# Kernel tuning notes

Hardware: AMD Instinct MI355X
Metric: run time of the kernel (lower is better)

Reference implementation:

```python
import jax, jax.numpy as jnp
import numpy as np

B = 8
H1c = W1c = 56
H2c = W2c = 112
C1 = 512
C2 = 256
NH = 8
WS = 7
POOL = 2
EPS = 1e-5


def setup_inputs() -> dict:
    key = jax.random.key(0)
    ks = jax.random.split(key, 8)
    x = jax.random.normal(ks[0], (B, H1c * W1c, C1), dtype=jnp.float32)
    y = jax.random.normal(ks[1], (B, H2c * W2c, C2), dtype=jnp.float32)
    Wq = jax.random.normal(ks[2], (C1, C1), dtype=jnp.float32) * 0.02
    Wkv = jax.random.normal(ks[3], (2 * C1, C2), dtype=jnp.float32) * 0.02
    Wproj = jax.random.normal(ks[4], (C1, C1), dtype=jnp.float32) * 0.02
    bproj = jnp.zeros((C1,), dtype=jnp.float32)
    # 1x1 conv: fan_out = out_channels -> std = sqrt(2/C2)
    Wsr = jax.random.normal(ks[5], (C2, C2), dtype=jnp.float32) * np.sqrt(2.0 / C2).astype(np.float32)
    bsr = jnp.zeros((C2,), dtype=jnp.float32)
    gn = jnp.ones((C2,), dtype=jnp.float32)
    bn = jnp.zeros((C2,), dtype=jnp.float32)
    return {"x": x, "y": y, "Wq": Wq, "Wkv": Wkv, "Wproj": Wproj,
            "bproj": bproj, "Wsr": Wsr, "bsr": bsr, "gn": gn, "bn": bn,
            "H1": H1c, "W1": W1c, "H2": H2c, "W2": W2c}


def _window_partition(t, ws):
    # t: (B, nh, H, W, C) -> (B*nh, num_windows, ws*ws, C)
    Bt, n, H, W, C = t.shape
    ht, wt = H // ws, W // ws
    t = t.reshape(Bt, n, ht, ws, wt, ws, C).transpose(0, 1, 2, 4, 3, 5, 6)
    return t.reshape(Bt * n, ht * wt, ws * ws, C)


def reference(x, y, Wq, Wkv, Wproj, bproj, Wsr, bsr, gn, bn, H1, W1, H2, W2):
    B1, N1, c1 = x.shape
    B2, N2, c2 = y.shape
    nh, ws = NH, WS
    hd = c1 // nh
    scale = hd ** (-0.5)

    # q projection -> (B, nh, H1, W1, hd)
    q = (x @ Wq.T).reshape(B1, H1, W1, nh, hd).transpose(0, 3, 1, 2, 4)

    # KV preprocessing: avgpool -> 1x1 conv -> layernorm -> gelu
    y2 = y.transpose(0, 2, 1).reshape(B2, c2, H2, W2)
    Hp, Wp = H2 // POOL, W2 // POOL
    y2 = y2.reshape(B2, c2, Hp, POOL, Wp, POOL).mean(axis=(3, 5))
    y2 = jnp.einsum('bchw,oc->bohw', y2, Wsr) + bsr[None, :, None, None]
    y2 = y2.reshape(B2, c2, Hp * Wp).transpose(0, 2, 1)  # (B, Np, C2)
    mu = y2.mean(-1, keepdims=True)
    var = y2.var(-1, keepdims=True)
    y2 = (y2 - mu) / jnp.sqrt(var + EPS) * gn + bn
    y2 = jax.nn.gelu(y2, approximate=False)

    kv = (y2 @ Wkv.T).reshape(B2, Hp * Wp, 2, nh, hd)
    k = kv[:, :, 0].transpose(0, 2, 1, 3).reshape(B2, nh, Hp, Wp, hd)
    v = kv[:, :, 1].transpose(0, 2, 1, 3).reshape(B2, nh, Hp, Wp, hd)

    qw = _window_partition(q, ws)   # (B*nh, nw, ws^2, hd)
    kw = _window_partition(k, ws)
    vw = _window_partition(v, ws)

    attn = jax.nn.softmax(jnp.einsum('bnqd,bnkd->bnqk', qw, kw) * scale, axis=-1)
    out = jnp.einsum('bnqk,bnkd->bnqd', attn, vw)  # (B*nh, nw, ws^2, hd)

    # window reverse -> (B, N1, C1)
    ht, wt = H1 // ws, W1 // ws
    out = out.reshape(B1, nh, ht, wt, ws, ws, hd).transpose(0, 1, 2, 4, 3, 5, 6)
    out = out.reshape(B1, nh, H1 * W1, hd).transpose(0, 2, 1, 3).reshape(B1, H1 * W1, c1)
    return out @ Wproj.T + bproj
```

## Files before the change

### kernel.cpp

```cpp
#include <hip/hip_runtime.h>
#include <hip/hip_bf16.h>

typedef __attribute__((ext_vector_type(8))) short short8;
typedef __attribute__((ext_vector_type(4))) float f32x4;
typedef __attribute__((ext_vector_type(4))) unsigned short ushort4v;

#define DI __device__ __forceinline__

DI unsigned short f2bf(float f) {
  union { float f; unsigned int u; } a; a.f = f;
  unsigned int u = a.u;
  return (unsigned short)((u + 0x7FFFu + ((u >> 16) & 1u)) >> 16);
}

#define BARRIER() do { asm volatile("" ::: "memory"); __builtin_amdgcn_s_barrier(); asm volatile("" ::: "memory"); } while (0)
#define GLOAD16(src, dst) __builtin_amdgcn_global_load_lds( \
    (const __attribute__((address_space(1))) void*)(src), \
    (__attribute__((address_space(3))) void*)(dst), 16, 0, 0)


__global__ __launch_bounds__(256)
void cvt_pool(const float* __restrict__ y, unsigned short* __restrict__ pooled,
              const float* __restrict__ Wq, const float* __restrict__ Wkv,
              const float* __restrict__ Wproj, const float* __restrict__ Wsr,
              unsigned short* __restrict__ Wq_b, unsigned short* __restrict__ Wkv_b,
              unsigned short* __restrict__ Wproj_b, unsigned short* __restrict__ Wsr_b) {
  int bid = blockIdx.x;
  if (bid < 6272) {
    int t = bid * 256 + threadIdx.x;
    int cv = (t & 63) * 4;
    int bp = t >> 6;
    int b = bp / 3136, p = bp % 3136;
    int hp = p / 56, wp = p % 56;
    const float* src = y + (((size_t)b * 12544) + hp * 224 + wp * 2) * 256 + cv;
    float4 a0 = *(const float4*)(src);
    float4 a1 = *(const float4*)(src + 256);
    float4 a2 = *(const float4*)(src + 28672);
    float4 a3 = *(const float4*)(src + 28672 + 256);
    float4 av;
    av.x = (a0.x + a1.x + a2.x + a3.x) * 0.25f;
    av.y = (a0.y + a1.y + a2.y + a3.y) * 0.25f;
    av.z = (a0.z + a1.z + a2.z + a3.z) * 0.25f;
    av.w = (a0.w + a1.w + a2.w + a3.w) * 0.25f;
    ushort4v o = { f2bf(av.x), f2bf(av.y), f2bf(av.z), f2bf(av.w) };
    *(ushort4v*)&pooled[(size_t)bp * 256 + cv] = o;
  } else {
    long i = (long)(bid - 6272) * 1024 + threadIdx.x * 4;
    const float* src; unsigned short* dst; long off;
    if (i < 262144L)      { src = Wq;    dst = Wq_b;    off = i; }
    else if (i < 524288L) { src = Wkv;   dst = Wkv_b;   off = i - 262144L; }
    else if (i < 786432L) { src = Wproj; dst = Wproj_b; off = i - 524288L; }
    else                  { src = Wsr;   dst = Wsr_b;   off = i - 786432L; }
    float4 v = *(const float4*)&src[off];
    ushort4v o = { f2bf(v.x), f2bf(v.y), f2bf(v.z), f2bf(v.w) };
    *(ushort4v*)&dst[off] = o;
  }
}

__global__ __launch_bounds__(256)
void sr_gemm(const unsigned short* __restrict__ Ap, const unsigned short* __restrict__ Wsr_b,
             const float* __restrict__ bsr, const float* __restrict__ gn,
             const float* __restrict__ bn, unsigned short* __restrict__ out) {
  __shared__ unsigned short sA[64 * 64];
  __shared__ unsigned short sB[256 * 64];
  __shared__ float red[64 * 8];

  const int tid = threadIdx.x;
  const int wv = tid >> 6;
  const int lane = tid & 63;
  const int lr = lane & 15;
  const int lg = lane >> 4;
  const int lr4 = lg * 4;
  const int m0 = blockIdx.x * 64;
  const int sr8 = lane >> 3;
  const int sl8 = lane & 7;

  f32x4 acc[4][4];
#pragma unroll
  for (int i = 0; i < 4; ++i)
#pragma unroll
    for (int j = 0; j < 4; ++j) acc[i][j] = (f32x4){0.f, 0.f, 0.f, 0.f};

  for (int kt = 0; kt < 256; kt += 64) {
#pragma unroll
    for (int c = 0; c < 2; ++c) {
      int row = wv * 16 + c * 8 + sr8;
      GLOAD16(Ap + (size_t)(m0 + row) * 256 + kt + ((sl8 ^ (row & 7)) * 8),
              &sA[(wv * 16 + c * 8) * 64]);
    }
#pragma unroll
    for (int c = 0; c < 8; ++c) {
      int row = wv * 64 + c * 8 + sr8;
      GLOAD16(Wsr_b + (size_t)row * 256 + kt + ((sl8 ^ (row & 7)) * 8),
              &sB[(wv * 64 + c * 8) * 64]);
    }
    __syncthreads();
#pragma unroll
    for (int ks = 0; ks < 2; ++ks) {
      short8 af[4], bfr[4];
#pragma unroll
      for (int i = 0; i < 4; ++i)
        af[i] = *(const short8*)&sA[(i * 16 + lr) * 64 + (((ks * 4 + lg) ^ (lr & 7)) * 8)];
#pragma unroll
      for (int j = 0; j < 4; ++j)
        bfr[j] = *(const short8*)&sB[(wv * 64 + j * 16 + lr) * 64 + (((ks * 4 + lg) ^ (lr & 7)) * 8)];
#pragma unroll
      for (int i = 0; i < 4; ++i)
#pragma unroll
        for (int j = 0; j < 4; ++j)
          acc[i][j] = __builtin_amdgcn_mfma_f32_16x16x32_bf16(af[i], bfr[j], acc[i][j], 0, 0, 0);
    }
    __syncthreads();
  }

  float bsv[4], gnv[4], bnv[4];
#pragma unroll
  for (int j = 0; j < 4; ++j) {
    int col = wv * 64 + j * 16 + lr;
    bsv[j] = bsr[col]; gnv[j] = gn[col]; bnv[j] = bn[col];
  }
  float s_[4][4], q_[4][4];
#pragma unroll
  for (int i = 0; i < 4; ++i)
#pragma unroll
    for (int r = 0; r < 4; ++r) {
      float s = 0.f, q = 0.f;
#pragma unroll
      for (int j = 0; j < 4; ++j) {
        float v = acc[i][j][r] + bsv[j];
        acc[i][j][r] = v;
        s += v; q += v * v;
      }
      s_[i][r] = s; q_[i][r] = q;
    }
#pragma unroll
  for (int m = 1; m <= 8; m <<= 1)
#pragma unroll
    for (int i = 0; i < 4; ++i)
#pragma unroll
      for (int r = 0; r < 4; ++r) {
        s_[i][r] += __shfl_xor(s_[i][r], m);
        q_[i][r] += __shfl_xor(q_[i][r], m);
      }
  if (lr == 0) {
#pragma unroll
    for (int i = 0; i < 4; ++i)
#pragma unroll
      for (int r = 0; r < 4; ++r) {
        int row = i * 16 + lr4 + r;
        red[row * 8 + wv * 2 + 0] = s_[i][r];
        red[row * 8 + wv * 2 + 1] = q_[i][r];
      }
  }
  __syncthreads();
#pragma unroll
  for (int i = 0; i < 4; ++i) {
#pragma unroll
    for (int r = 0; r < 4; ++r) {
      int row = i * 16 + lr4 + r;
      float sum = red[row * 8 + 0] + red[row * 8 + 2] + red[row * 8 + 4] + red[row * 8 + 6];
      float sq  = red[row * 8 + 1] + red[row * 8 + 3] + red[row * 8 + 5] + red[row * 8 + 7];
      float mean = sum * (1.f / 256.f);
      float var = sq * (1.f / 256.f) - mean * mean;
      float rstd = rsqrtf(var + 1e-5f);
#pragma unroll
      for (int j = 0; j < 4; ++j) {
        float t = (acc[i][j][r] - mean) * rstd * gnv[j] + bnv[j];
        t = 0.5f * t * (1.f + erff(t * 0.70710678118654752f));
        out[(size_t)(m0 + row) * 256 + wv * 64 + j * 16 + lr] = f2bf(t);
      }
    }
  }
}

DI void epi_q(int gm, int gc, float v, unsigned short* outp) {
  const int b = gm / 3136, pos = gm % 3136;
  const int h = pos / 56, ww = pos % 56;
  const int head = gc >> 6, d = gc & 63;
  const size_t idx = ((((size_t)(b * 8 + head)) * 64 + (h / 7) * 8 + (ww / 7)) * 49
                      + (h % 7) * 7 + (ww % 7)) * 64 + d;
  outp[idx] = f2bf(v);
}

template<int K, int N>
__global__ __launch_bounds__(512, 2)
void gemm256f(const float* __restrict__ A,
              const unsigned short* __restrict__ Bw,
              unsigned short* __restrict__ outp) {
  __shared__ unsigned short lds[65536];
  const int tid = threadIdx.x;
  const int wv = tid >> 6;
  const int lane = tid & 63;
  const int wm = wv >> 2;
  const int wn = wv & 3;
  const int m0 = blockIdx.y * 256;
  const int n0 = blockIdx.x * 256;
  const int lr = lane & 15;
  const int lg = lane >> 4;
  const int lr4 = lg * 4;
  const int srow8 = lane >> 3;
  const int sl8 = lane & 7;
  constexpr int NT = K / 64;

  f32x4 acc[8][4];
#pragma unroll
  for (int i = 0; i < 8; ++i)
#pragma unroll
    for (int j = 0; j < 4; ++j) acc[i][j] = (f32x4){0.f, 0.f, 0.f, 0.f};

  float4 fa[4][2];
  auto loadA = [&](int t1) {
    int tsrc = (t1 < NT) ? t1 : NT - 1;
#pragma unroll
    for (int rr = 0; rr < 4; ++rr) {
      int trow = rr * 64 + wv * 8 + srow8;
      const float* p = A + (size_t)(m0 + trow) * K + tsrc * 64 + sl8 * 8;
      fa[rr][0] = *(const float4*)p;
      fa[rr][1] = *(const float4*)(p + 4);
    }
    asm volatile("" ::: "memory");
  };
  auto writeA = [&](int t1) {
#pragma unroll
    for (int rr = 0; rr < 4; ++rr) {
      int trow = rr * 64 + wv * 8 + srow8;
      union { short8 s; unsigned short u[8]; } w;
      w.u[0] = f2bf(fa[rr][0].x); w.u[1] = f2bf(fa[rr][0].y);
      w.u[2] = f2bf(fa[rr][0].z); w.u[3] = f2bf(fa[rr][0].w);
      w.u[4] = f2bf(fa[rr][1].x); w.u[5] = f2bf(fa[rr][1].y);
      w.u[6] = f2bf(fa[rr][1].z); w.u[7] = f2bf(fa[rr][1].w);
      *(short8*)&lds[(t1 & 1) * 32768 + trow * 64 + ((sl8 ^ (trow & 7)) * 8)] = w.s;
    }
  };
  auto stageB = [&](int t1, int rr) {
    int tsrc = (t1 < NT) ? t1 : NT - 1;
    int trow = rr * 64 + wv * 8 + srow8;
    int sx = sl8 ^ (trow & 7);
    GLOAD16(Bw + (size_t)(n0 + trow) * K + tsrc * 64 + sx * 8,
            &lds[(t1 & 1) * 32768 + 16384 + (rr * 64 + wv * 8) * 64]);
  };
  auto rdA = [&](int s, int mf, int ks) -> short8 {
    int row = wm * 128 + mf * 16 + lr;
    int slot = ((ks << 2) + lg) ^ (row & 7);
    return *(const short8*)&lds[s * 32768 + row * 64 + slot * 8];
  };
  auto rdB = [&](int s, int nf, int ks) -> short8 {
    int row = wn * 64 + nf * 16 + lr;
    int slot = ((ks << 2) + lg) ^ (row & 7);
    return *(const short8*)&lds[s * 32768 + 16384 + row * 64 + slot * 8];
  };

  stageB(0, 0); stageB(0, 1); stageB(0, 2); stageB(0, 3);
  loadA(0);
  asm volatile("s_waitcnt vmcnt(0)" ::: "memory");
  writeA(0);
  asm volatile("s_waitcnt lgkmcnt(0)" ::: "memory");
  BARRIER();

  for (int t = 0; t < NT; ++t) {
    const int s = t & 1;
    short8 bfr[4][2];
    loadA(t + 1);
#pragma unroll
    for (int j = 0; j < 4; ++j) { bfr[j][0] = rdB(s, j, 0); bfr[j][1] = rdB(s, j, 1); }
    {
      short8 x0 = rdA(s, 0, 0), x1 = rdA(s, 0, 1);
      short8 y0 = rdA(s, 1, 0), y1 = rdA(s, 1, 1);
      BARRIER();
      __builtin_amdgcn_s_setprio(1);
#pragma unroll
      for (int j = 0; j < 4; ++j) {
        acc[0][j] = __builtin_amdgcn_mfma_f32_16x16x32_bf16(x0, bfr[j][0], acc[0][j], 0, 0, 0);
        acc[0][j] = __builtin_amdgcn_mfma_f32_16x16x32_bf16(x1, bfr[j][1], acc[0][j], 0, 0, 0);
        acc[1][j] = __builtin_amdgcn_mfma_f32_16x16x32_bf16(y0, bfr[j][0], acc[1][j], 0, 0, 0);
        acc[1][j] = __builtin_amdgcn_mfma_f32_16x16x32_bf16(y1, bfr[j][1], acc[1][j], 0, 0, 0);
      }
      __builtin_amdgcn_s_setprio(0);
      BARRIER();
    }
    stageB(t + 1, 0); stageB(t + 1, 1);
    {
      short8 x0 = rdA(s, 2, 0), x1 = rdA(s, 2, 1);
      short8 y0 = rdA(s, 3, 0), y1 = rdA(s, 3, 1);
      BARRIER();
      __builtin_amdgcn_s_setprio(1);
#pragma unroll
      for (int j = 0; j < 4; ++j) {
        acc[2][j] = __builtin_amdgcn_mfma_f32_16x16x32_bf16(x0, bfr[j][0], acc[2][j], 0, 0, 0);
        acc[2][j] = __builtin_amdgcn_mfma_f32_16x16x32_bf16(x1, bfr[j][1], acc[2][j], 0, 0, 0);
        acc[3][j] = __builtin_amdgcn_mfma_f32_16x16x32_bf16(y0, bfr[j][0], acc[3][j], 0, 0, 0);
        acc[3][j] = __builtin_amdgcn_mfma_f32_16x16x32_bf16(y1, bfr[j][1], acc[3][j], 0, 0, 0);
      }
      __builtin_amdgcn_s_setprio(0);
      BARRIER();
    }
    stageB(t + 1, 2); stageB(t + 1, 3);
    {
      short8 x0 = rdA(s, 4, 0), x1 = rdA(s, 4, 1);
      short8 y0 = rdA(s, 5, 0), y1 = rdA(s, 5, 1);
      BARRIER();
      __builtin_amdgcn_s_setprio(1);
#pragma unroll
      for (int j = 0; j < 4; ++j) {
        acc[4][j] = __builtin_amdgcn_mfma_f32_16x16x32_bf16(x0, bfr[j][0], acc[4][j], 0, 0, 0);
        acc[4][j] = __builtin_amdgcn_mfma_f32_16x16x32_bf16(x1, bfr[j][1], acc[4][j], 0, 0, 0);
        acc[5][j] = __builtin_amdgcn_mfma_f32_16x16x32_bf16(y0, bfr[j][0], acc[5][j], 0, 0, 0);
        acc[5][j] = __builtin_amdgcn_mfma_f32_16x16x32_bf16(y1, bfr[j][1], acc[5][j], 0, 0, 0);
      }
      __builtin_amdgcn_s_setprio(0);
      BARRIER();
    }
    {
      short8 x0 = rdA(s, 6, 0), x1 = rdA(s, 6, 1);
      short8 y0 = rdA(s, 7, 0), y1 = rdA(s, 7, 1);
      asm volatile("s_waitcnt vmcnt(4)" ::: "memory");
      writeA(t + 1);
      asm volatile("s_waitcnt lgkmcnt(0)" ::: "memory");
      BARRIER();
      __builtin_amdgcn_s_setprio(1);
#pragma unroll
      for (int j = 0; j < 4; ++j) {
        acc[6][j] = __builtin_amdgcn_mfma_f32_16x16x32_bf16(x0, bfr[j][0], acc[6][j], 0, 0, 0);
        acc[6][j] = __builtin_amdgcn_mfma_f32_16x16x32_bf16(x1, bfr[j][1], acc[6][j], 0, 0, 0);
        acc[7][j] = __builtin_amdgcn_mfma_f32_16x16x32_bf16(y0, bfr[j][0], acc[7][j], 0, 0, 0);
        acc[7][j] = __builtin_amdgcn_mfma_f32_16x16x32_bf16(y1, bfr[j][1], acc[7][j], 0, 0, 0);
      }
      __builtin_amdgcn_s_setprio(0);
      asm volatile("s_waitcnt vmcnt(0)" ::: "memory");
      BARRIER();
    }
  }

#pragma unroll
  for (int i = 0; i < 8; ++i)
#pragma unroll
    for (int j = 0; j < 4; ++j)
#pragma unroll
      for (int r = 0; r < 4; ++r)
        epi_q(m0 + wm * 128 + i * 16 + lr4 + r, n0 + wn * 64 + j * 16 + lr,
              acc[i][j][r], outp);
}

__global__ __launch_bounds__(1024)
void kvattn(const unsigned short* __restrict__ y2,
            const unsigned short* __restrict__ Wkv_b,
            const unsigned short* __restrict__ qwin,
            const unsigned short* __restrict__ Wproj_b,
            const float* __restrict__ bproj,
            float* __restrict__ out) {
  __shared__ unsigned short lds[81920];
  const int tid = threadIdx.x;
  const int wv16 = tid >> 6;
  const int head = wv16 >> 1;
  const int half = wv16 & 1;
  const int lane = tid & 63;
  const int lr = lane & 15;
  const int lg = lane >> 4;
  const int r8 = lane >> 3;
  const int sl8 = lane & 7;
  const int bb = blockIdx.x >> 6;
  const int win = blockIdx.x & 63;
  const int ht = win >> 3, wt = win & 7;

  unsigned short* Cy  = lds;
  unsigned short* SLh = lds + 16384 + head * 8192;
  unsigned short* OA  = lds + 16384;
  unsigned short* WPs = lds + 49152 + wv16 * 2048;

  {
    int rb = wv16 & 7;
    int m = rb * 8 + r8;
    int mm = (m < 49) ? m : 48;
    int grow = bb * 3136 + (ht * 7 + mm / 7) * 56 + wt * 7 + (mm % 7);
    int p0 = wv16 >> 3;
#pragma unroll
    for (int pp = 0; pp < 2; ++pp) {
      int panel = p0 + pp * 2;
      GLOAD16(y2 + (size_t)grow * 256 + panel * 64 + ((sl8 ^ (m & 7)) * 8),
              &Cy[panel * 4096 + rb * 512]);
    }
  }

  auto stageW = [&](int s) {
    int h2 = s >> 2, kt = s & 3;
#pragma unroll
    for (int c = 0; c < 4; ++c) {
      int lrow = half * 32 + c * 8 + r8;
      GLOAD16(Wkv_b + (size_t)(h2 * 512 + head * 64 + lrow) * 256 + kt * 64 + ((sl8 ^ r8) * 8),
              &SLh[(s & 1) * 4096 + (half * 32 + c * 8) * 64]);
    }
  };

  f32x4 aK[4][2], aV[4][2];
#pragma unroll
  for (int i = 0; i < 4; ++i)
#pragma unroll
    for (int j = 0; j < 2; ++j) { aK[i][j] = (f32x4){0,0,0,0}; aV[i][j] = (f32x4){0,0,0,0}; }

  stageW(0);
  asm volatile("s_waitcnt vmcnt(4)" ::: "memory");
  BARRIER();

#pragma unroll
  for (int s = 0; s < 8; ++s) {
    if (s < 7) {
      stageW(s + 1);
      asm volatile("s_waitcnt vmcnt(4)" ::: "memory");
    } else {
      asm volatile("s_waitcnt vmcnt(0)" ::: "memory");
    }
    const int kt = s & 3;
    const unsigned short* Wb = &SLh[(s & 1) * 4096];
    short8 bfrg[2][2];
#pragma unroll
    for (int nf2 = 0; nf2 < 2; ++nf2)
#pragma unroll
      for (int ks = 0; ks < 2; ++ks) {
        int row = (half * 2 + nf2) * 16 + lr;
        bfrg[nf2][ks] = *(const short8*)&Wb[row * 64 + (((ks * 4 + lg) ^ (lr & 7)) * 8)];
      }
#pragma unroll
    for (int mf = 0; mf < 4; ++mf)
#pragma unroll
      for (int ks = 0; ks < 2; ++ks) {
        short8 af = *(const short8*)&Cy[kt * 4096 + (mf * 16 + lr) * 64 + (((ks * 4 + lg) ^ (lr & 7)) * 8)];
#pragma unroll
        for (int nf2 = 0; nf2 < 2; ++nf2) {
          if (s < 4)
            aK[mf][nf2] = __builtin_amdgcn_mfma_f32_16x16x32_bf16(af, bfrg[nf2][ks], aK[mf][nf2], 0, 0, 0);
          else
            aV[mf][nf2] = __builtin_amdgcn_mfma_f32_16x16x32_bf16(af, bfrg[nf2][ks], aV[mf][nf2], 0, 0, 0);
        }
      }
  }

  const unsigned short* qb = qwin + (size_t)((bb * 8 + head) * 64 + win) * 3136;
  short8 qf[2][2];
#pragma unroll
  for (int mf2 = 0; mf2 < 2; ++mf2)
#pragma unroll
    for (int ks = 0; ks < 2; ++ks)
      qf[mf2][ks] = *(const short8*)&qb[((half * 2 + mf2) * 16 + lr) * 64 + ks * 32 + lg * 8];

  BARRIER();

#pragma unroll
  for (int mf = 0; mf < 4; ++mf)
#pragma unroll
    for (int nf2 = 0; nf2 < 2; ++nf2)
#pragma unroll
      for (int r = 0; r < 4; ++r) {
        int key = mf * 16 + lg * 4 + r;
        int d = (half * 2 + nf2) * 16 + lr;
        SLh[key * 64 + (((d >> 3) ^ (key & 7)) * 8) + (d & 7)] = f2bf(aK[mf][nf2][r]);
        SLh[4096 + d * 64 + (((key >> 3) ^ (d & 7)) * 8) + (key & 7)] = f2bf(aV[mf][nf2][r]);
      }
  asm volatile("s_waitcnt lgkmcnt(0)" ::: "memory");
  BARRIER();

  f32x4 aS[2][4];
#pragma unroll
  for (int i = 0; i < 2; ++i)
#pragma unroll
    for (int j = 0; j < 4; ++j) aS[i][j] = (f32x4){0,0,0,0};
#pragma unroll
  for (int mf2 = 0; mf2 < 2; ++mf2)
#pragma unroll
    for (int ks = 0; ks < 2; ++ks)
#pragma unroll
      for (int nf = 0; nf < 4; ++nf) {
        short8 bk = *(const short8*)&SLh[(nf * 16 + lr) * 64 + (((ks * 4 + lg) ^ (lr & 7)) * 8)];
        aS[mf2][nf] = __builtin_amdgcn_mfma_f32_16x16x32_bf16(qf[mf2][ks], bk, aS[mf2][nf], 0, 0, 0);
      }

#pragma unroll
  for (int nf = 0; nf < 4; ++nf)
    if (nf * 16 + lr >= 49) {
#pragma unroll
      for (int mf2 = 0; mf2 < 2; ++mf2)
#pragma unroll
        for (int r = 0; r < 4; ++r) aS[mf2][nf][r] = -1e30f;
    }
  const float cexp = 0.125f * 1.4426950408889634f;
  float mx[2][4], sm[2][4];
#pragma unroll
  for (int mf2 = 0; mf2 < 2; ++mf2)
#pragma unroll
    for (int r = 0; r < 4; ++r)
      mx[mf2][r] = fmaxf(fmaxf(aS[mf2][0][r], aS[mf2][1][r]), fmaxf(aS[mf2][2][r], aS[mf2][3][r]));
#pragma unroll
  for (int m = 1; m <= 8; m <<= 1)
#pragma unroll
    for (int mf2 = 0; mf2 < 2; ++mf2)
#pragma unroll
      for (int r = 0; r < 4; ++r) mx[mf2][r] = fmaxf(mx[mf2][r], __shfl_xor(mx[mf2][r], m));
#pragma unroll
  for (int mf2 = 0; mf2 < 2; ++mf2)
#pragma unroll
    for (int nf = 0; nf < 4; ++nf)
#pragma unroll
      for (int r = 0; r < 4; ++r)
        aS[mf2][nf][r] = exp2f((aS[mf2][nf][r] - mx[mf2][r]) * cexp);
#pragma unroll
  for (int mf2 = 0; mf2 < 2; ++mf2)
#pragma unroll
    for (int r = 0; r < 4; ++r)
      sm[mf2][r] = aS[mf2][0][r] + aS[mf2][1][r] + aS[mf2][2][r] + aS[mf2][3][r];
#pragma unroll
  for (int m = 1; m <= 8; m <<= 1)
#pragma unroll
    for (int mf2 = 0; mf2 < 2; ++mf2)
#pragma unroll
      for (int r = 0; r < 4; ++r) sm[mf2][r] += __shfl_xor(sm[mf2][r], m);
#pragma unroll
  for (int mf2 = 0; mf2 < 2; ++mf2)
#pragma unroll
    for (int r = 0; r < 4; ++r) sm[mf2][r] = 1.f / sm[mf2][r];

  BARRIER();

#pragma unroll
  for (int mf2 = 0; mf2 < 2; ++mf2)
#pragma unroll
    for (int nf = 0; nf < 4; ++nf)
#pragma unroll
      for (int r = 0; r < 4; ++r) {
        int q = (half * 2 + mf2) * 16 + lg * 4 + r;
        int key = nf * 16 + lr;
        SLh[q * 64 + (((key >> 3) ^ (q & 7)) * 8) + (key & 7)] = f2bf(aS[mf2][nf][r] * sm[mf2][r]);
      }

  f32x4 aO[2][4];
#pragma unroll
  for (int i = 0; i < 2; ++i)
#pragma unroll
    for (int j = 0; j < 4; ++j) aO[i][j] = (f32x4){0,0,0,0};
#pragma unroll
  for (int mf2 = 0; mf2 < 2; ++mf2)
#pragma unroll
    for (int ks = 0; ks < 2; ++ks) {
      int qrow = (half * 2 + mf2) * 16 + lr;
      short8 pf = *(const short8*)&SLh[qrow * 64 + (((ks * 4 + lg) ^ (lr & 7)) * 8)];
#pragma unroll
      for (int df = 0; df < 4; ++df) {
        short8 vf = *(const short8*)&SLh[4096 + (df * 16 + lr) * 64 + (((ks * 4 + lg) ^ (lr & 7)) * 8)];
        aO[mf2][df] = __builtin_amdgcn_mfma_f32_16x16x32_bf16(pf, vf, aO[mf2][df], 0, 0, 0);
      }
    }

  BARRIER();

#pragma unroll
  for (int mf2 = 0; mf2 < 2; ++mf2)
#pragma unroll
    for (int df = 0; df < 4; ++df)
#pragma unroll
      for (int r = 0; r < 4; ++r) {
        int q = (half * 2 + mf2) * 16 + lg * 4 + r;
        int slot = df * 2 + (lr >> 3);
        OA[q * 512 + head * 64 + ((slot ^ (q & 7)) * 8) + (lr & 7)] = f2bf(aO[mf2][df][r]);
      }
#pragma unroll
  for (int c = 0; c < 4; ++c) {
    int lrow = c * 8 + r8;
    GLOAD16(Wproj_b + (size_t)(head * 64 + half * 32 + lrow) * 512 + ((sl8 ^ r8) * 8),
            &WPs[c * 512]);
  }
  asm volatile("s_waitcnt lgkmcnt(0) vmcnt(0)" ::: "memory");
  BARRIER();

  f32x4 aR[4][2];
#pragma unroll
  for (int i = 0; i < 4; ++i)
#pragma unroll
    for (int j = 0; j < 2; ++j) aR[i][j] = (f32x4){0,0,0,0};
#pragma unroll
  for (int kt = 0; kt < 8; ++kt) {
    short8 nx[4];
    if (kt < 7) {
#pragma unroll
      for (int c = 0; c < 4; ++c) {
        int lrow = c * 8 + r8;
        nx[c] = *(const short8*)&Wproj_b[(size_t)(head * 64 + half * 32 + lrow) * 512
                                         + (kt + 1) * 64 + ((sl8 ^ r8) * 8)];
      }
    }
#pragma unroll
    for (int mf = 0; mf < 4; ++mf)
#pragma unroll
      for (int ks = 0; ks < 2; ++ks) {
        short8 af = *(const short8*)&OA[(mf * 16 + lr) * 512 + kt * 64 + (((ks * 4 + lg) ^ (lr & 7)) * 8)];
#pragma unroll
        for (int nf2 = 0; nf2 < 2; ++nf2) {
          short8 bf2 = *(const short8*)&WPs[(nf2 * 16 + lr) * 64 + (((ks * 4 + lg) ^ (lr & 7)) * 8)];
          aR[mf][nf2] = __builtin_amdgcn_mfma_f32_16x16x32_bf16(af, bf2, aR[mf][nf2], 0, 0, 0);
        }
      }
    if (kt < 7) {
#pragma unroll
      for (int c = 0; c < 4; ++c)
        *(short8*)&WPs[(c * 8 + r8) * 64 + sl8 * 8] = nx[c];
    }
  }

#pragma unroll
  for (int mf = 0; mf < 4; ++mf)
#pragma unroll
    for (int nf2 = 0; nf2 < 2; ++nf2)
#pragma unroll
      for (int r = 0; r < 4; ++r) {
        int q = mf * 16 + lg * 4 + r;
        if (q < 49) {
          int gm = bb * 3136 + (ht * 7 + q / 7) * 56 + wt * 7 + (q % 7);
          int col = head * 64 + (half * 2 + nf2) * 16 + lr;
          out[(size_t)gm * 512 + col] = aR[mf][nf2][r] + bproj[col];
        }
      }
}

extern "C" void kernel_launch(void* const* d_in, const int* in_sizes, int n_in,
                              void* d_out, int out_size, void* d_ws, size_t ws_size,
                              hipStream_t stream) {
  const float* x     = (const float*)d_in[0];
  const float* y     = (const float*)d_in[1];
  const float* Wq    = (const float*)d_in[2];
  const float* Wkv   = (const float*)d_in[3];
  const float* Wproj = (const float*)d_in[4];
  const float* bproj = (const float*)d_in[5];
  const float* Wsr   = (const float*)d_in[6];
  const float* bsr   = (const float*)d_in[7];
  const float* gn    = (const float*)d_in[8];
  const float* bn    = (const float*)d_in[9];
  float* out = (float*)d_out;

  char* ws = (char*)d_ws;
  unsigned short* Wq_b    = (unsigned short*)ws; ws += 524288;
  unsigned short* Wkv_b   = (unsigned short*)ws; ws += 524288;
  unsigned short* Wproj_b = (unsigned short*)ws; ws += 524288;
  unsigned short* Wsr_b   = (unsigned short*)ws; ws += 131072;
  unsigned short* regA    = (unsigned short*)ws; ws += 12845056;
  unsigned short* q_win   = (unsigned short*)ws; ws += 25690112;
  unsigned short* regC    = (unsigned short*)ws; ws += 12845056;

  cvt_pool<<<7104, 256, 0, stream>>>(y, regA, Wq, Wkv, Wproj, Wsr,
                                     Wq_b, Wkv_b, Wproj_b, Wsr_b);

  gemm256f<512, 512><<<dim3(2, 98), 512, 0, stream>>>(x, Wq_b, q_win);

  sr_gemm<<<392, 256, 0, stream>>>(regA, Wsr_b, bsr, gn, bn, regC);

  kvattn<<<512, 1024, 0, stream>>>(regC, Wkv_b, q_win, Wproj_b, bproj, out);
}
```

Before: 139.8 us.

## Load Wkv and Wproj fragments directly from global instead of LDS staging

The KV projection and output projection now read weight B-fragments straight from global memory (and L2) into registers, replacing the double-buffered global-to-LDS staging of Wkv and the LDS staging of Wproj. The KV loop is reordered so each A tile from LDS is reused for both the K and V halves, and the OA buffer is moved to overlay the Cy region. This drops LDS traffic, several barriers and LDS footprint, which may help occupancy. In exchange the weight loads are no longer swizzled or coalesced through LDS and their global latency sits directly on the MFMA path.

```diff
diff --git a/kernel.cpp b/kernel.cpp
--- a/kernel.cpp
+++ b/kernel.cpp
@@ -364,8 +364,7 @@
 
   unsigned short* Cy  = lds;
   unsigned short* SLh = lds + 16384 + head * 8192;
-  unsigned short* OA  = lds + 16384;
-  unsigned short* WPs = lds + 49152 + wv16 * 2048;
+  unsigned short* OA  = lds;
 
   {
     int rb = wv16 & 7;
@@ -380,16 +379,8 @@
               &Cy[panel * 4096 + rb * 512]);
     }
   }
-
-  auto stageW = [&](int s) {
-    int h2 = s >> 2, kt = s & 3;
-#pragma unroll
-    for (int c = 0; c < 4; ++c) {
-      int lrow = half * 32 + c * 8 + r8;
-      GLOAD16(Wkv_b + (size_t)(h2 * 512 + head * 64 + lrow) * 256 + kt * 64 + ((sl8 ^ r8) * 8),
-              &SLh[(s & 1) * 4096 + (half * 32 + c * 8) * 64]);
-    }
-  };
+  asm volatile("s_waitcnt vmcnt(0)" ::: "memory");
+  BARRIER();
 
   f32x4 aK[4][2], aV[4][2];
 #pragma unroll
@@ -397,41 +388,36 @@
 #pragma unroll
     for (int j = 0; j < 2; ++j) { aK[i][j] = (f32x4){0,0,0,0}; aV[i][j] = (f32x4){0,0,0,0}; }
 
-  stageW(0);
-  asm volatile("s_waitcnt vmcnt(4)" ::: "memory");
-  BARRIER();
-
-#pragma unroll
-  for (int s = 0; s < 8; ++s) {
-    if (s < 7) {
-      stageW(s + 1);
-      asm volatile("s_waitcnt vmcnt(4)" ::: "memory");
-    } else {
-      asm volatile("s_waitcnt vmcnt(0)" ::: "memory");
-    }
-    const int kt = s & 3;
-    const unsigned short* Wb = &SLh[(s & 1) * 4096];
-    short8 bfrg[2][2];
-#pragma unroll
-    for (int nf2 = 0; nf2 < 2; ++nf2)
-#pragma unroll
-      for (int ks = 0; ks < 2; ++ks) {
-        int row = (half * 2 + nf2) * 16 + lr;
-        bfrg[nf2][ks] = *(const short8*)&Wb[row * 64 + (((ks * 4 + lg) ^ (lr & 7)) * 8)];
-      }
+  const int wrow = head * 64 + half * 32;
+#pragma unroll
+  for (int kt = 0; kt < 4; ++kt) {
+    short8 af[4][2];
 #pragma unroll
     for (int mf = 0; mf < 4; ++mf)
 #pragma unroll
-      for (int ks = 0; ks < 2; ++ks) {
-        short8 af = *(const short8*)&Cy[kt * 4096 + (mf * 16 + lr) * 64 + (((ks * 4 + lg) ^ (lr & 7)) * 8)];
-#pragma unroll
-        for (int nf2 = 0; nf2 < 2; ++nf2) {
-          if (s < 4)
-            aK[mf][nf2] = __builtin_amdgcn_mfma_f32_16x16x32_bf16(af, bfrg[nf2][ks], aK[mf][nf2], 0, 0, 0);
-          else
-            aV[mf][nf2] = __builtin_amdgcn_mfma_f32_16x16x32_bf16(af, bfrg[nf2][ks], aV[mf][nf2], 0, 0, 0);
-        }
-      }
+      for (int ks = 0; ks < 2; ++ks)
+        af[mf][ks] = *(const short8*)&Cy[kt * 4096 + (mf * 16 + lr) * 64 + (((ks * 4 + lg) ^ (lr & 7)) * 8)];
+#pragma unroll
+    for (int h2 = 0; h2 < 2; ++h2) {
+      short8 bfrg[2][2];
+#pragma unroll
+      for (int nf2 = 0; nf2 < 2; ++nf2)
+#pragma unroll
+        for (int ks = 0; ks < 2; ++ks)
+          bfrg[nf2][ks] = *(const short8*)&Wkv_b[(size_t)(h2 * 512 + wrow + nf2 * 16 + lr) * 256
+                                                 + kt * 64 + (ks * 4 + lg) * 8];
+#pragma unroll
+      for (int mf = 0; mf < 4; ++mf)
+#pragma unroll
+        for (int ks = 0; ks < 2; ++ks)
+#pragma unroll
+          for (int nf2 = 0; nf2 < 2; ++nf2) {
+            if (h2 == 0)
+              aK[mf][nf2] = __builtin_amdgcn_mfma_f32_16x16x32_bf16(af[mf][ks], bfrg[nf2][ks], aK[mf][nf2], 0, 0, 0);
+            else
+              aV[mf][nf2] = __builtin_amdgcn_mfma_f32_16x16x32_bf16(af[mf][ks], bfrg[nf2][ks], aV[mf][nf2], 0, 0, 0);
+          }
+    }
   }
 
   const unsigned short* qb = qwin + (size_t)((bb * 8 + head) * 64 + win) * 3136;
@@ -441,8 +427,6 @@
 #pragma unroll
     for (int ks = 0; ks < 2; ++ks)
       qf[mf2][ks] = *(const short8*)&qb[((half * 2 + mf2) * 16 + lr) * 64 + ks * 32 + lg * 8];
-
-  BARRIER();
 
 #pragma unroll
   for (int mf = 0; mf < 4; ++mf)
@@ -560,13 +544,7 @@
         int slot = df * 2 + (lr >> 3);
         OA[q * 512 + head * 64 + ((slot ^ (q & 7)) * 8) + (lr & 7)] = f2bf(aO[mf2][df][r]);
       }
-#pragma unroll
-  for (int c = 0; c < 4; ++c) {
-    int lrow = c * 8 + r8;
-    GLOAD16(Wproj_b + (size_t)(head * 64 + half * 32 + lrow) * 512 + ((sl8 ^ r8) * 8),
-            &WPs[c * 512]);
-  }
-  asm volatile("s_waitcnt lgkmcnt(0) vmcnt(0)" ::: "memory");
+  asm volatile("s_waitcnt lgkmcnt(0)" ::: "memory");
   BARRIER();
 
   f32x4 aR[4][2];
@@ -576,30 +554,20 @@
     for (int j = 0; j < 2; ++j) aR[i][j] = (f32x4){0,0,0,0};
 #pragma unroll
   for (int kt = 0; kt < 8; ++kt) {
-    short8 nx[4];
-    if (kt < 7) {
-#pragma unroll
-      for (int c = 0; c < 4; ++c) {
-        int lrow = c * 8 + r8;
-        nx[c] = *(const short8*)&Wproj_b[(size_t)(head * 64 + half * 32 + lrow) * 512
-                                         + (kt + 1) * 64 + ((sl8 ^ r8) * 8)];
-      }
-    }
-#pragma unroll
-    for (int mf = 0; mf < 4; ++mf)
-#pragma unroll
-      for (int ks = 0; ks < 2; ++ks) {
+#pragma unroll
+    for (int ks = 0; ks < 2; ++ks) {
+      short8 bf2[2];
+#pragma unroll
+      for (int nf2 = 0; nf2 < 2; ++nf2)
+        bf2[nf2] = *(const short8*)&Wproj_b[(size_t)(wrow + nf2 * 16 + lr) * 512
+                                            + kt * 64 + (ks * 4 + lg) * 8];
+#pragma unroll
+      for (int mf = 0; mf < 4; ++mf) {
         short8 af = *(const short8*)&OA[(mf * 16 + lr) * 512 + kt * 64 + (((ks * 4 + lg) ^ (lr & 7)) * 8)];
 #pragma unroll
-        for (int nf2 = 0; nf2 < 2; ++nf2) {
-          short8 bf2 = *(const short8*)&WPs[(nf2 * 16 + lr) * 64 + (((ks * 4 + lg) ^ (lr & 7)) * 8)];
-          aR[mf][nf2] = __builtin_amdgcn_mfma_f32_16x16x32_bf16(af, bf2, aR[mf][nf2], 0, 0, 0);
-        }
-      }
-    if (kt < 7) {
-#pragma unroll
-      for (int c = 0; c < 4; ++c)
-        *(short8*)&WPs[(c * 8 + r8) * 64 + sl8 * 8] = nx[c];
+        for (int nf2 = 0; nf2 < 2; ++nf2)
+          aR[mf][nf2] = __builtin_amdgcn_mfma_f32_16x16x32_bf16(af, bf2[nf2], aR[mf][nf2], 0, 0, 0);
+      }
     }
   }
 
@@ -612,7 +580,7 @@
         int q = mf * 16 + lg * 4 + r;
         if (q < 49) {
           int gm = bb * 3136 + (ht * 7 + q / 7) * 56 + wt * 7 + (q % 7);
-          int col = head * 64 + (half * 2 + nf2) * 16 + lr;
+          int col = wrow + nf2 * 16 + lr;
           out[(size_t)gm * 512 + col] = aR[mf][nf2][r] + bproj[col];
         }
       }
```

Result: slower. 173.2 us (+23.8%).
